# Performance work log

Hardware: AMD Instinct MI355X
Metric: run time of the kernel (lower is better)

The kernel has to match this reference:

```python
import jax, jax.numpy as jnp
import numpy as np

WS = 16          # window_size
SHIFT = 8        # shift_size
HEADS = 6
DIM = 180
CONV_SCALE = 0.01
EPS = 1e-5       # LayerNorm eps (torch default)


def _ln(x, g, b):
    mu = jnp.mean(x, -1, keepdims=True)
    var = jnp.mean((x - mu) ** 2, -1, keepdims=True)
    return (x - mu) / jnp.sqrt(var + EPS) * g + b


def _window_partition(x, ws):
    b, h, w, c = x.shape
    x = x.reshape(b, h // ws, ws, w // ws, ws, c)
    return x.transpose(0, 1, 3, 2, 4, 5).reshape(-1, ws, ws, c)


def _window_reverse(win, ws, h, w):
    b = win.shape[0] // ((h // ws) * (w // ws))
    x = win.reshape(b, h // ws, w // ws, ws, ws, -1)
    return x.transpose(0, 1, 3, 2, 4, 5).reshape(b, h, w, -1)


def _conv2d(x, w, b, pad):
    y = jax.lax.conv_general_dilated(x, w, (1, 1), ((pad, pad), (pad, pad)),
                                     dimension_numbers=('NCHW', 'OIHW', 'NCHW'))
    return y + b[None, :, None, None]


def setup_inputs() -> dict:
    key = jax.random.key(0)
    ks = jax.random.split(key, 12)
    b, h, w = 1, 256, 256
    c = DIM
    hid = int(c * 4.0)
    cr = c // 3     # compress_ratio=3
    sq = c // 30    # squeeze_factor=30
    x = jax.random.normal(ks[0], (b, h * w, c), jnp.float32)

    # relative position index (standard Swin recipe)
    coords = np.stack(np.meshgrid(np.arange(WS), np.arange(WS), indexing='ij')).reshape(2, -1)
    rel = (coords[:, :, None] - coords[:, None, :]).transpose(1, 2, 0)
    rel[:, :, 0] += WS - 1
    rel[:, :, 1] += WS - 1
    rel[:, :, 0] *= 2 * WS - 1
    rpi_sa = jnp.asarray(rel.sum(-1), jnp.int32)  # [ws*ws, ws*ws]

    # shifted-window attention mask
    img = np.zeros((h, w))
    cnt = 0
    for hs in (slice(0, -WS), slice(-WS, -SHIFT), slice(-SHIFT, None)):
        for wsl in (slice(0, -WS), slice(-WS, -SHIFT), slice(-SHIFT, None)):
            img[hs, wsl] = cnt
            cnt += 1
    mw = img.reshape(h // WS, WS, w // WS, WS).transpose(0, 2, 1, 3).reshape(-1, WS * WS)
    am = mw[:, None, :] - mw[:, :, None]
    attn_mask = jnp.asarray(np.where(am != 0, -100.0, 0.0), jnp.float32)  # [nW, n, n]

    def p(k, shape, std=0.02):
        return jax.random.normal(k, shape, jnp.float32) * std

    return dict(
        x=x, h=h, w=w, rpi_sa=rpi_sa, attn_mask=attn_mask,
        norm1_g=jnp.ones((c,), jnp.float32), norm1_b=jnp.zeros((c,), jnp.float32),
        qkv_w=p(ks[1], (c, 3 * c)), qkv_b=jnp.zeros((3 * c,), jnp.float32),
        rpb_table=p(ks[2], ((2 * WS - 1) * (2 * WS - 1), HEADS)),
        proj_w=p(ks[3], (c, c)), proj_b=jnp.zeros((c,), jnp.float32),
        conv1_w=p(ks[4], (cr, c, 3, 3)), conv1_b=jnp.zeros((cr,), jnp.float32),
        conv2_w=p(ks[5], (c, cr, 3, 3)), conv2_b=jnp.zeros((c,), jnp.float32),
        ca1_w=p(ks[6], (sq, c, 1, 1)), ca1_b=jnp.zeros((sq,), jnp.float32),
        ca2_w=p(ks[7], (c, sq, 1, 1)), ca2_b=jnp.zeros((c,), jnp.float32),
        norm2_g=jnp.ones((c,), jnp.float32), norm2_b=jnp.zeros((c,), jnp.float32),
        fc1_w=p(ks[8], (c, hid)), fc1_b=jnp.zeros((hid,), jnp.float32),
        fc2_w=p(ks[9], (hid, c)), fc2_b=jnp.zeros((c,), jnp.float32),
    )


def reference(x, h, w, rpi_sa, attn_mask,
              norm1_g, norm1_b, qkv_w, qkv_b, rpb_table, proj_w, proj_b,
              conv1_w, conv1_b, conv2_w, conv2_b, ca1_w, ca1_b, ca2_w, ca2_b,
              norm2_g, norm2_b, fc1_w, fc1_b, fc2_w, fc2_b):
    b, _, c = x.shape
    shortcut = x
    xn = _ln(x, norm1_g, norm1_b).reshape(b, h, w, c)

    # CAB conv branch (NCHW)
    xi = xn.transpose(0, 3, 1, 2)
    y = _conv2d(xi, conv1_w, conv1_b, 1)
    y = jax.nn.gelu(y, approximate=False)
    y = _conv2d(y, conv2_w, conv2_b, 1)
    ca = jnp.mean(y, axis=(2, 3), keepdims=True)          # AdaptiveAvgPool2d(1)
    ca = jax.nn.relu(_conv2d(ca, ca1_w, ca1_b, 0))
    ca = jax.nn.sigmoid(_conv2d(ca, ca2_w, ca2_b, 0))
    conv_x = (y * ca).transpose(0, 2, 3, 1).reshape(b, h * w, c)

    # shifted window attention
    sx = jnp.roll(xn, (-SHIFT, -SHIFT), (1, 2))
    xw = _window_partition(sx, WS).reshape(-1, WS * WS, c)  # [B_, n, c]
    B_, n, _ = xw.shape
    hd = c // HEADS
    qkv = (xw @ qkv_w + qkv_b).reshape(B_, n, 3, HEADS, hd).transpose(2, 0, 3, 1, 4)
    q, k, v = qkv[0] * hd ** (-0.5), qkv[1], qkv[2]
    attn = jnp.einsum('bhqd,bhkd->bhqk', q, k)
    rpb = rpb_table[rpi_sa.reshape(-1)].reshape(n, n, HEADS).transpose(2, 0, 1)
    attn = attn + rpb[None]
    nw = attn_mask.shape[0]
    attn = attn.reshape(B_ // nw, nw, HEADS, n, n) + attn_mask[None, :, None]
    attn = jax.nn.softmax(attn.reshape(B_, HEADS, n, n), -1)
    out = jnp.einsum('bhqk,bhkd->bhqd', attn, v).transpose(0, 2, 1, 3).reshape(B_, n, c)
    out = out @ proj_w + proj_b
    sx = _window_reverse(out.reshape(-1, WS, WS, c), WS, h, w)
    attn_x = jnp.roll(sx, (SHIFT, SHIFT), (1, 2)).reshape(b, h * w, c)

    x = shortcut + attn_x + conv_x * CONV_SCALE
    xm = _ln(x, norm2_g, norm2_b)
    m = jax.nn.gelu(xm @ fc1_w + fc1_b, approximate=False)
    x = x + (m @ fc2_w + fc2_b)
    return x
```

## Files before the change

### kernel.cpp

```cpp
#include <hip/hip_runtime.h>
#include <hip/hip_bf16.h>
#include <math.h>

#define NTOK 65536
#define C 180
#define KP1 192
#define RCHUNK 32768
#define LOG2E 1.4426950408889634f

typedef __attribute__((ext_vector_type(8))) __bf16 bf16x8;
typedef __attribute__((ext_vector_type(4))) float floatx4;

__device__ __forceinline__ float gelu_f(float v) {
    return 0.5f * v * (1.f + erff(v * 0.7071067811865475f));
}
__device__ __forceinline__ float bflo(unsigned int u) { return __uint_as_float(u << 16); }
__device__ __forceinline__ float bfhi(unsigned int u) { return __uint_as_float(u & 0xffff0000u); }

__device__ __forceinline__ void async_copy16(const unsigned short* g, unsigned short* l) {
    __builtin_amdgcn_global_load_lds(
        (const __attribute__((address_space(1))) unsigned int*)g,
        (__attribute__((address_space(3))) unsigned int*)l, 16, 0, 0);
}

__device__ __forceinline__ int win2pix(int wrow) {
    int wi = wrow >> 8, ni = wrow & 255;
    int r2 = ((wi >> 4) << 4) | (ni >> 4);
    int c2 = ((wi & 15) << 4) | (ni & 15);
    int r = (r2 + 8) & 255, c = (c2 + 8) & 255;
    return (r << 8) | c;
}

__global__ __launch_bounds__(256) void ln_k(const float* __restrict__ x,
                                            const float* __restrict__ g,
                                            const float* __restrict__ b,
                                            __hip_bfloat16* __restrict__ y) {
    const int wav = threadIdx.x >> 6;
    const int lane = threadIdx.x & 63;
    const int row = blockIdx.x * 4 + wav;
    const float* xr = x + (size_t)row * C;
    float v0 = xr[lane];
    float v1 = xr[lane + 64];
    float v2 = (lane < C - 128) ? xr[lane + 128] : 0.f;
    float sum = v0 + v1 + v2;
    float sq = v0 * v0 + v1 * v1 + v2 * v2;
#pragma unroll
    for (int off = 32; off >= 1; off >>= 1) {
        sum += __shfl_xor(sum, off, 64);
        sq += __shfl_xor(sq, off, 64);
    }
    const float mu = sum * (1.f / C);
    const float var = sq * (1.f / C) - mu * mu;
    const float rstd = rsqrtf(var + 1e-5f);
    __hip_bfloat16* yr = y + (size_t)row * KP1;
#pragma unroll
    for (int e = 0; e < 3; ++e) {
        int col = lane + 64 * e;
        float val = 0.f;
        if (col < C) {
            float vv = (e == 0) ? v0 : (e == 1 ? v1 : v2);
            val = (vv - mu) * rstd * g[col] + b[col];
        }
        yr[col] = __float2bfloat16(val);
    }
}

__device__ __forceinline__ void wconv_item(const float* __restrict__ w,
                                           __hip_bfloat16* __restrict__ wb,
                                           int O, int I, int OCP, int KP, int idx) {
    int tap = idx / (OCP * KP);
    int rem = idx - tap * (OCP * KP);
    int oc = rem / KP, ch = rem - oc * KP;
    float v = (oc < O && ch < I) ? w[((size_t)(oc * I + ch)) * 9 + tap] : 0.f;
    wb[idx] = __float2bfloat16(v);
}
__device__ __forceinline__ void wprep_item(const float* __restrict__ w,
                                           __hip_bfloat16* __restrict__ bt,
                                           int K, int N, int KPd, int idx) {
    int n = idx / KPd, k = idx - n * KPd;
    float v = (n < N && k < K) ? w[(size_t)k * N + n] : 0.f;
    bt[idx] = __float2bfloat16(v);
}
__global__ void prep_all_k(const int* __restrict__ rpi, const float* __restrict__ table,
                           const float* __restrict__ mask,
                           __hip_bfloat16* __restrict__ rpbM,
                           const float* __restrict__ c1w, __hip_bfloat16* __restrict__ wb1,
                           const float* __restrict__ c2w, __hip_bfloat16* __restrict__ wb2,
                           const float* __restrict__ qkvw, __hip_bfloat16* __restrict__ qkvbt,
                           const float* __restrict__ projw, __hip_bfloat16* __restrict__ projbt,
                           const float* __restrict__ f1w, __hip_bfloat16* __restrict__ f1bt,
                           const float* __restrict__ f2w, __hip_bfloat16* __restrict__ f2bt) {
    int idx = blockIdx.x * 256 + threadIdx.x;
    if (idx < 65536) {
        int t = rpi[idx];
        float m1 = mask[(size_t)15 * 65536 + idx];
        float m2 = mask[(size_t)240 * 65536 + idx];
        float m3 = mask[(size_t)255 * 65536 + idx];
#pragma unroll
        for (int h = 0; h < 6; ++h) {
            float base = table[t * 6 + h];
            rpbM[((size_t)(0 * 6 + h)) * 65536 + idx] = __float2bfloat16(base * LOG2E);
            rpbM[((size_t)(1 * 6 + h)) * 65536 + idx] = __float2bfloat16((base + m1) * LOG2E);
            rpbM[((size_t)(2 * 6 + h)) * 65536 + idx] = __float2bfloat16((base + m2) * LOG2E);
            rpbM[((size_t)(3 * 6 + h)) * 65536 + idx] = __float2bfloat16((base + m3) * LOG2E);
        }
        return;
    }
    idx -= 65536;
    if (idx < 110592) { wconv_item(c1w, wb1, 60, 180, 64, 192, idx); return; }
    idx -= 110592;
    if (idx < 110592) { wconv_item(c2w, wb2, 180, 60, 192, 64, idx); return; }
    idx -= 110592;
    if (idx < 122880) { wprep_item(qkvw, qkvbt, 180, 540, 192, idx); return; }
    idx -= 122880;
    if (idx < 36864) { wprep_item(projw, projbt, 180, 180, 192, idx); return; }
    idx -= 36864;
    if (idx < 147456) { wprep_item(f1w, f1bt, 180, 720, 192, idx); return; }
    idx -= 147456;
    if (idx < 147456) { wprep_item(f2w, f2bt, 720, 180, 768, idx); return; }
}

template <int TH, int CINP, int COUT, int OSTR, int ACT, int OUTBF>
__global__ __launch_bounds__(256) void mconv_k(const __hip_bfloat16* __restrict__ in, int istr,
                                               const __hip_bfloat16* __restrict__ wb,
                                               const float* __restrict__ bias,
                                               void* __restrict__ outp) {
    constexpr int MI = TH / 4;
    __shared__ __hip_bfloat16 sP[(TH + 2) * 18 * 40];
    __shared__ __hip_bfloat16 sW[9 * 64 * 40];
    const int tid = threadIdx.x;
    const int tr0 = (blockIdx.x >> 4) * TH, tc0 = (blockIdx.x & 15) * 16;
    const int ocbase = blockIdx.y * 64;
    const int w = tid >> 6, lane = tid & 63, fr = lane & 15, q = lane >> 4;
    constexpr int OCP = ((COUT + 63) / 64) * 64;
    floatx4 acc[MI][4] = {};
    for (int c0 = 0; c0 < CINP; c0 += 32) {
        for (int l = tid; l < (TH + 2) * 18 * 4; l += 256) {
            int pos = l >> 2, part = l & 3;
            int pr = pos / 18, pc = pos - pr * 18;
            int gr = tr0 + pr - 1, gc = tc0 + pc - 1;
            float4 v = make_float4(0.f, 0.f, 0.f, 0.f);
            if (gr >= 0 && gr < 256 && gc >= 0 && gc < 256)
                v = *(const float4*)(in + (size_t)(gr * 256 + gc) * istr + c0 + part * 8);
            *(float4*)(sP + pos * 40 + part * 8) = v;
        }
        for (int l = tid; l < 9 * 64 * 4; l += 256) {
            int part = l & 3, oc = (l >> 2) & 63, tap = l >> 8;
            *(float4*)(sW + tap * 2560 + oc * 40 + part * 8) =
                *(const float4*)(wb + (size_t)(tap * OCP + ocbase + oc) * CINP + c0 + part * 8);
        }
        __syncthreads();
#pragma unroll
        for (int tap = 0; tap < 9; ++tap) {
            const int dy = tap / 3, dx = tap - 3 * (tap / 3);
            bf16x8 af[MI], bw[4];
#pragma unroll
            for (int mi = 0; mi < MI; ++mi) {
                int pr = MI * w + mi + dy, pc = fr + dx;
                af[mi] = *(const bf16x8*)(sP + (pr * 18 + pc) * 40 + q * 8);
            }
#pragma unroll
            for (int nj = 0; nj < 4; ++nj)
                bw[nj] = *(const bf16x8*)(sW + tap * 2560 + (nj * 16 + fr) * 40 + q * 8);
#pragma unroll
            for (int mi = 0; mi < MI; ++mi)
#pragma unroll
                for (int nj = 0; nj < 4; ++nj)
                    acc[mi][nj] =
                        __builtin_amdgcn_mfma_f32_16x16x32_bf16(af[mi], bw[nj], acc[mi][nj], 0, 0, 0);
        }
        __syncthreads();
    }
#pragma unroll
    for (int mi = 0; mi < MI; ++mi) {
#pragma unroll
        for (int r = 0; r < 4; ++r) {
            const int irow = tr0 + MI * w + mi;
            const int icol = tc0 + q * 4 + r;
            const size_t obase = (size_t)(irow * 256 + icol) * OSTR + ocbase;
#pragma unroll
            for (int nj = 0; nj < 4; ++nj) {
                int oc = ocbase + nj * 16 + fr;
                float bv = (oc < COUT) ? bias[oc] : 0.f;
                float v = acc[mi][nj][r] + bv;
                if (ACT) v = gelu_f(v);
                if (OUTBF) {
                    ((__hip_bfloat16*)outp)[obase + nj * 16 + fr] = __float2bfloat16(v);
                } else {
                    if (oc < COUT) ((float*)outp)[obase + nj * 16 + fr] = v;
                }
            }
        }
    }
}

__global__ __launch_bounds__(192) void chansum_k(const float* __restrict__ y2,
                                                 float* __restrict__ partials) {
    const int tid = threadIdx.x;
    if (tid >= C) return;
    const size_t base = (size_t)blockIdx.x * 256 * C;
    float s = 0.f;
    for (int p = 0; p < 256; ++p) s += y2[base + (size_t)p * C + tid];
    partials[blockIdx.x * C + tid] = s;
}

__global__ __launch_bounds__(256) void ca_k(const float* __restrict__ partials,
                                            const float* __restrict__ w1, const float* __restrict__ b1,
                                            const float* __restrict__ w2, const float* __restrict__ b2,
                                            float* __restrict__ scale) {
    __shared__ float mean[C];
    __shared__ float s1[6];
    const int tid = threadIdx.x;
    if (tid < C) {
        float s = 0.f;
        for (int b_ = 0; b_ < 256; ++b_) s += partials[b_ * C + tid];
        mean[tid] = s * (1.f / 65536.f);
    }
    __syncthreads();
    if (tid < 6) {
        float s = b1[tid];
        for (int ch = 0; ch < C; ++ch) s += mean[ch] * w1[tid * C + ch];
        s1[tid] = fmaxf(s, 0.f);
    }
    __syncthreads();
    if (tid < C) {
        float s = b2[tid];
#pragma unroll
        for (int j = 0; j < 6; ++j) s += s1[j] * w2[tid * 6 + j];
        scale[tid] = 1.f / (1.f + __expf(-s));
    }
}

template <int MODE, int BN>
__global__ __launch_bounds__(256) void mgemm_k(const unsigned short* __restrict__ A,
                                               const unsigned short* __restrict__ BT,
                                               const float* __restrict__ bias,
                                               const float* __restrict__ xres,
                                               const float* __restrict__ scale,
                                               void* __restrict__ Cout,
                                               int KPd, int N, int cstride, int rowoff) {
    __shared__ unsigned short As[128 * 32];
    __shared__ unsigned short Bs[BN * 32];
    constexpr int NJ = BN / 32;
    const int tid = threadIdx.x;
    const int m0 = blockIdx.x * 128, n0 = blockIdx.y * BN;
    const int wave = tid >> 6, lane = tid & 63;
    const int wm = (wave & 1) * 64, wn = (wave >> 1) * (BN / 2);
    const int fr = lane & 15, q = lane >> 4;
    const int subrow = lane >> 2;
    const int chunk = (lane & 3) ^ (subrow & 3);

    const int rl0 = wave * 16 + subrow;
    const int rl1 = (wave + 4) * 16 + subrow;
    size_t abase0, abase1;
    if (MODE == 3) {
        abase0 = (size_t)win2pix(rowoff + m0 + rl0) * KPd + chunk * 8;
        abase1 = (size_t)win2pix(rowoff + m0 + rl1) * KPd + chunk * 8;
    } else if (MODE == 5) {
        abase0 = (size_t)(m0 + rl0) * 32 + chunk * 8;
        abase1 = (size_t)(m0 + rl1) * 32 + chunk * 8;
    } else {
        abase0 = (size_t)(m0 + rl0) * KPd + chunk * 8;
        abase1 = (size_t)(m0 + rl1) * KPd + chunk * 8;
    }
    const size_t bbase0 = (size_t)(n0 + rl0) * KPd + chunk * 8;
    const size_t bbase1 = (size_t)(n0 + rl1) * KPd + chunk * 8;

    floatx4 acc[4][NJ] = {};
    for (int k0 = 0; k0 < KPd; k0 += 32) {
        if (MODE == 5) {
            const size_t kofs = (size_t)(k0 >> 5) * cstride * 32;
            async_copy16(A + kofs + abase0, As + wave * 512);
            async_copy16(A + kofs + abase1, As + (wave + 4) * 512);
        } else {
            async_copy16(A + abase0 + k0, As + wave * 512);
            async_copy16(A + abase1 + k0, As + (wave + 4) * 512);
        }
        async_copy16(BT + bbase0 + k0, Bs + wave * 512);
        if (BN == 128) async_copy16(BT + bbase1 + k0, Bs + (wave + 4) * 512);
        __syncthreads();
        bf16x8 af[4], fB[NJ];
        const int sw = (q ^ (fr & 3)) << 4;
#pragma unroll
        for (int i = 0; i < 4; ++i)
            af[i] = *(const bf16x8*)((const char*)As + (wm + i * 16 + fr) * 64 + sw);
#pragma unroll
        for (int j = 0; j < NJ; ++j)
            fB[j] = *(const bf16x8*)((const char*)Bs + (wn + j * 16 + fr) * 64 + sw);
#pragma unroll
        for (int i = 0; i < 4; ++i)
#pragma unroll
            for (int j = 0; j < NJ; ++j)
                acc[i][j] = __builtin_amdgcn_mfma_f32_16x16x32_bf16(af[i], fB[j], acc[i][j], 0, 0, 0);
        __syncthreads();
    }
#pragma unroll
    for (int i = 0; i < 4; ++i) {
#pragma unroll
        for (int r = 0; r < 4; ++r) {
            const int grow = m0 + wm + i * 16 + q * 4 + r;
            int pix = 0;
            if (MODE == 5) pix = win2pix(rowoff + grow);
#pragma unroll
            for (int j = 0; j < NJ; ++j) {
                const int col = n0 + wn + j * 16 + fr;
                float v = acc[i][j][r];
                if (MODE == 1 || MODE == 3) {
                    if (col < cstride) {
                        float vv = 0.f;
                        if (col < N) {
                            vv = v + bias[col];
                            if (MODE == 1) vv = gelu_f(vv);
                        }
                        ((__hip_bfloat16*)Cout)[(size_t)grow * cstride + col] = __float2bfloat16(vv);
                    }
                } else if (MODE == 2) {
                    if (col < N) {
                        float* o = (float*)Cout;
                        size_t ix = (size_t)grow * 180 + col;
                        o[ix] = v + bias[col] + xres[ix];
                    }
                } else if (MODE == 5) {
                    if (col < N) {
                        float* o = (float*)Cout;
                        size_t ix = (size_t)pix * 180 + col;
                        o[ix] = xres[ix] + v + bias[col] + o[ix] * scale[col] * 0.01f;
                    }
                }
            }
        }
    }
}

__global__ __launch_bounds__(256, 4) void attn12_k(const __hip_bfloat16* __restrict__ qkv,
                                                   const __hip_bfloat16* __restrict__ rpbM,
                                                   __hip_bfloat16* __restrict__ attn_out,
                                                   int wbase, int rows) {
    const int wl = blockIdx.x, h = blockIdx.y;
    const int wig = wbase + wl;
    const int typ = (((wig >> 4) == 15) ? 2 : 0) + (((wig & 15) == 15) ? 1 : 0);
    const int tid = threadIdx.x;
    const int w = tid >> 6, lane = tid & 63;
    const int fr = lane & 15, q = lane >> 4;
    __shared__ __hip_bfloat16 kk[256 * 32];
    __shared__ __hip_bfloat16 vT[32 * 256];

    union UB2 { unsigned int u; __hip_bfloat162 h2; };
    union U8 { unsigned int u[4]; bf16x8 v; };

    const int rowbase = wl * 256 + w * 64;
    bf16x8 qf[4];
#pragma unroll
    for (int qi = 0; qi < 4; ++qi) {
        const unsigned int* p32 =
            (const unsigned int*)(qkv + (size_t)(rowbase + qi * 16 + fr) * 576 + h * 30);
        U8 t;
#pragma unroll
        for (int jj = 0; jj < 4; ++jj) t.u[jj] = p32[q * 4 + jj];
        qf[qi] = t.v;
    }

    const __hip_bfloat16* rpbh = rpbM + ((size_t)(typ * 6 + h)) * 65536;
    uint2 rb[4][4];
#pragma unroll
    for (int qi = 0; qi < 4; ++qi) {
        const size_t qoff = ((size_t)(w * 64 + qi * 16 + fr)) * 256 + q * 4;
#pragma unroll
        for (int ki = 0; ki < 4; ++ki)
            rb[qi][ki] = *(const uint2*)(rpbh + qoff + ki * 16);
    }

    for (int l = tid; l < 256 * 15; l += 256) {
        int key = l / 15, dw_ = l - key * 15;
        const unsigned int* ks =
            (const unsigned int*)(qkv + (size_t)(wl * 256 + key) * 576 + 180 + h * 30);
        unsigned int kv = ks[dw_];
        *(unsigned int*)((char*)kk + key * 64 + (((dw_ >> 2) ^ (key & 3)) << 4) + ((dw_ & 3) << 2)) = kv;
        UB2 vv; vv.u = ks[90 + dw_];
        const int d0 = 2 * dw_, d1 = d0 + 1;
        *(__hip_bfloat16*)((char*)vT + d0 * 512 + (((key >> 3) ^ d0) << 4) + ((key & 7) << 1)) = vv.h2.x;
        *(__hip_bfloat16*)((char*)vT + d1 * 512 + (((key >> 3) ^ d1) << 4) + ((key & 7) << 1)) = vv.h2.y;
    }
    *(unsigned int*)((char*)kk + tid * 64 + ((3 ^ (tid & 3)) << 4) + 12) = 0u;
    for (int l = tid; l < 2 * 256; l += 256) {
        int d = 30 + (l >> 8), key = l & 255;
        *(__hip_bfloat16*)((char*)vT + d * 512 + (((key >> 3) ^ d) << 4) + ((key & 7) << 1)) =
            __float2bfloat16(0.f);
    }
    __syncthreads();

    const float SC2 = 0.26339891239045137f;
    float lsum[4] = {};
    floatx4 o_[4][2] = {};
    const int srcA = fr + ((q & 1) << 5);
    const int srcB = srcA + 16;

#pragma unroll
    for (int nc = 0; nc < 4; ++nc) {
        if (nc > 0) {
#pragma unroll
            for (int qi = 0; qi < 4; ++qi) {
                const size_t qoff = ((size_t)(w * 64 + qi * 16 + fr)) * 256 + nc * 64 + q * 4;
#pragma unroll
                for (int ki = 0; ki < 4; ++ki)
                    rb[qi][ki] = *(const uint2*)(rpbh + qoff + ki * 16);
            }
        }
        bf16x8 kf[4];
#pragma unroll
        for (int ki = 0; ki < 4; ++ki) {
            const int key = nc * 64 + ki * 16 + fr;
            kf[ki] = *(const bf16x8*)((const char*)kk + key * 64 + ((q ^ (fr & 3)) << 4));
        }
        unsigned int dw[4][4][2];
#pragma unroll
        for (int qi = 0; qi < 4; ++qi) {
            floatx4 s_[4] = {};
#pragma unroll
            for (int ki = 0; ki < 4; ++ki)
                s_[ki] = __builtin_amdgcn_mfma_f32_16x16x32_bf16(kf[ki], qf[qi], s_[ki], 0, 0, 0);
#pragma unroll
            for (int ki = 0; ki < 4; ++ki) {
                uint2 rbv = rb[qi][ki];
                float b0 = bflo(rbv.x), b1 = bfhi(rbv.x), b2 = bflo(rbv.y), b3 = bfhi(rbv.y);
                float p0 = exp2f(fmaf(s_[ki][0], SC2, b0));
                float p1 = exp2f(fmaf(s_[ki][1], SC2, b1));
                float p2 = exp2f(fmaf(s_[ki][2], SC2, b2));
                float p3 = exp2f(fmaf(s_[ki][3], SC2, b3));
                lsum[qi] += (p0 + p1) + (p2 + p3);
                __hip_bfloat162 lo = {__float2bfloat16(p0), __float2bfloat16(p1)};
                __hip_bfloat162 hi = {__float2bfloat16(p2), __float2bfloat16(p3)};
                UB2 ul, uh; ul.h2 = lo; uh.h2 = hi;
                dw[ki][qi][0] = ul.u;
                dw[ki][qi][1] = uh.u;
            }
        }
#pragma unroll
        for (int kc = 0; kc < 2; ++kc) {
            bf16x8 pa[4];
#pragma unroll
            for (int mi = 0; mi < 4; ++mi) {
                unsigned g0 = __shfl((int)dw[2 * kc][mi][0], srcA, 64);
                unsigned g1 = __shfl((int)dw[2 * kc][mi][1], srcA, 64);
                unsigned g2 = __shfl((int)dw[2 * kc][mi][0], srcB, 64);
                unsigned g3 = __shfl((int)dw[2 * kc][mi][1], srcB, 64);
                unsigned h0 = __shfl((int)dw[2 * kc + 1][mi][0], srcA, 64);
                unsigned h1 = __shfl((int)dw[2 * kc + 1][mi][1], srcA, 64);
                unsigned h2 = __shfl((int)dw[2 * kc + 1][mi][0], srcB, 64);
                unsigned h3 = __shfl((int)dw[2 * kc + 1][mi][1], srcB, 64);
                U8 t;
                const bool lo = (q < 2);
                t.u[0] = lo ? g0 : h0;
                t.u[1] = lo ? g1 : h1;
                t.u[2] = lo ? g2 : h2;
                t.u[3] = lo ? g3 : h3;
                pa[mi] = t.v;
            }
            bf16x8 vb[2];
#pragma unroll
            for (int dj = 0; dj < 2; ++dj) {
                const int d = dj * 16 + fr;
                vb[dj] = *(const bf16x8*)((const char*)vT + d * 512 +
                                          (((nc * 8 + kc * 4 + q) ^ d) << 4));
            }
#pragma unroll
            for (int mi = 0; mi < 4; ++mi)
#pragma unroll
                for (int dj = 0; dj < 2; ++dj)
                    o_[mi][dj] =
                        __builtin_amdgcn_mfma_f32_16x16x32_bf16(pa[mi], vb[dj], o_[mi][dj], 0, 0, 0);
        }
    }
#pragma unroll
    for (int qi = 0; qi < 4; ++qi) {
        lsum[qi] += __shfl_xor(lsum[qi], 16, 64);
        lsum[qi] += __shfl_xor(lsum[qi], 32, 64);
    }
    __hip_bfloat16* plane = attn_out + (size_t)h * rows * 32;
#pragma unroll
    for (int mi = 0; mi < 4; ++mi) {
#pragma unroll
        for (int r = 0; r < 4; ++r) {
            float tot = __shfl(lsum[mi], q * 4 + r, 64);
            float inv = 1.f / tot;
            const int row_local = rowbase + mi * 16 + q * 4 + r;
            __hip_bfloat16* orow = plane + (size_t)row_local * 32;
#pragma unroll
            for (int dj = 0; dj < 2; ++dj) {
                int d = dj * 16 + fr;
                float val = (d < 30) ? o_[mi][dj][r] * inv : 0.f;
                orow[d] = __float2bfloat16(val);
            }
        }
    }
}

extern "C" void kernel_launch(void* const* d_in, const int* in_sizes, int n_in, void* d_out,
                              int out_size, void* d_ws, size_t ws_size, hipStream_t stream) {
    (void)in_sizes; (void)n_in; (void)out_size;
    const float* x = (const float*)d_in[0];
    const int* rpi = (const int*)d_in[3];
    const float* mask = (const float*)d_in[4];
    const float* n1g = (const float*)d_in[5];
    const float* n1b = (const float*)d_in[6];
    const float* qkvw = (const float*)d_in[7];
    const float* qkvb = (const float*)d_in[8];
    const float* rpbt = (const float*)d_in[9];
    const float* projw = (const float*)d_in[10];
    const float* projb = (const float*)d_in[11];
    const float* c1w = (const float*)d_in[12];
    const float* c1b = (const float*)d_in[13];
    const float* c2w = (const float*)d_in[14];
    const float* c2b = (const float*)d_in[15];
    const float* ca1w = (const float*)d_in[16];
    const float* ca1b = (const float*)d_in[17];
    const float* ca2w = (const float*)d_in[18];
    const float* ca2b = (const float*)d_in[19];
    const float* n2g = (const float*)d_in[20];
    const float* n2b = (const float*)d_in[21];
    const float* f1w = (const float*)d_in[22];
    const float* f1b = (const float*)d_in[23];
    const float* f2w = (const float*)d_in[24];
    const float* f2b = (const float*)d_in[25];

    float* ws = (float*)d_ws;
    float* out = (float*)d_out;

    const int merged = (ws_size >= 130511616ull) ? 1 : 0;
    const int RATT = merged ? 65536 : 32768;
    const int nck = merged ? 1 : 2;
    const size_t bufCf = merged ? 25165824u : 12582912u;
    const size_t attnCoff = merged ? 18874368u : 9437184u;

    float* xn_f     = ws;
    float* bufC     = xn_f + 6291456;
    float* partials = bufC + bufCf;
    float* scalep   = partials + 46080;
    float* rpbM_f   = scalep + 192;
    float* wb1_f    = rpbM_f + 786432;
    float* wb2_f    = wb1_f + 55296;
    float* qkvbt_f  = wb2_f + 55296;
    float* projbt_f = qkvbt_f + 61440;
    float* f1bt_f   = projbt_f + 18432;
    float* f2bt_f   = f1bt_f + 73728;

    __hip_bfloat16* xn    = (__hip_bfloat16*)xn_f;
    __hip_bfloat16* y1b   = (__hip_bfloat16*)bufC;
    __hip_bfloat16* qkvC  = (__hip_bfloat16*)bufC;
    __hip_bfloat16* attnC = (__hip_bfloat16*)(bufC + attnCoff);
    __hip_bfloat16* h1    = (__hip_bfloat16*)bufC;
    __hip_bfloat16* rpbM   = (__hip_bfloat16*)rpbM_f;
    __hip_bfloat16* wb1    = (__hip_bfloat16*)wb1_f;
    __hip_bfloat16* wb2    = (__hip_bfloat16*)wb2_f;
    __hip_bfloat16* qkvbt  = (__hip_bfloat16*)qkvbt_f;
    __hip_bfloat16* projbt = (__hip_bfloat16*)projbt_f;
    __hip_bfloat16* f1bt   = (__hip_bfloat16*)f1bt_f;
    __hip_bfloat16* f2bt   = (__hip_bfloat16*)f2bt_f;

    prep_all_k<<<(741376 + 255) / 256, 256, 0, stream>>>(rpi, rpbt, mask, rpbM, c1w, wb1, c2w, wb2,
                                                         qkvw, qkvbt, projw, projbt,
                                                         f1w, f1bt, f2w, f2bt);

    ln_k<<<NTOK / 4, 256, 0, stream>>>(x, n1g, n1b, xn);

    mconv_k<8, 192, 60, 64, 1, 1><<<dim3(512, 1), 256, 0, stream>>>(xn, 192, wb1, c1b, y1b);
    mconv_k<16, 64, 180, 180, 0, 0><<<dim3(256, 3), 256, 0, stream>>>(y1b, 64, wb2, c2b, out);
    chansum_k<<<256, 192, 0, stream>>>(out, partials);
    ca_k<<<1, 256, 0, stream>>>(partials, ca1w, ca1b, ca2w, ca2b, scalep);

    for (int ck = 0; ck < nck; ++ck) {
        const int rowoff = ck * RATT;
        mgemm_k<3, 128><<<dim3(RATT / 128, 5), 256, 0, stream>>>(
            (const unsigned short*)xn, (const unsigned short*)qkvbt, qkvb, nullptr, nullptr,
            qkvC, 192, 540, 576, rowoff);
        attn12_k<<<dim3(RATT / 256, 6), 256, 0, stream>>>(qkvC, rpbM, attnC, rowoff / 256, RATT);
        mgemm_k<5, 64><<<dim3(RATT / 128, 3), 256, 0, stream>>>(
            (const unsigned short*)attnC, (const unsigned short*)projbt, projb, x, scalep,
            out, 192, 180, RATT, rowoff);
    }

    ln_k<<<NTOK / 4, 256, 0, stream>>>(out, n2g, n2b, xn);

    const int nmlp = merged ? 1 : 2;
    const int RM = merged ? NTOK : RCHUNK;
    for (int ck = 0; ck < nmlp; ++ck) {
        const int rowoff = ck * RM;
        mgemm_k<1, 128><<<dim3(RM / 128, 6), 256, 0, stream>>>(
            (const unsigned short*)(xn + (size_t)rowoff * KP1), (const unsigned short*)f1bt,
            f1b, nullptr, nullptr, h1, 192, 720, 768, 0);
        mgemm_k<2, 64><<<dim3(RM / 128, 3), 256, 0, stream>>>(
            (const unsigned short*)h1, (const unsigned short*)f2bt, f2b,
            out + (size_t)rowoff * 180, nullptr, out + (size_t)rowoff * 180, 768, 180, 180, 0);
    }
}
```

Baseline: 686.9 us.

## Fuse MLP fc1+GELU+fc2 into one kernel keeping hidden tile in LDS

Replaces the two MLP GEMM launches (fc1 with GELU writing a 65536x768 bf16 hidden buffer, then fc2 with residual) with a single fused kernel. Each 128-row block loads its normalized input tile into LDS, computes 128-column hidden chunks with GELU into an LDS buffer, and accumulates fc2 directly, so the hidden activation never touches global memory. In exchange, the grid shrinks to 512 blocks with large LDS use (about 80KB) and heavy register use for two accumulator sets. Weight fragments are read straight from global memory with no LDS staging, which may stall the MFMA pipeline.

```diff
diff --git a/kernel.cpp b/kernel.cpp
--- a/kernel.cpp
+++ b/kernel.cpp
@@ -5,7 +5,6 @@
 #define NTOK 65536
 #define C 180
 #define KP1 192
-#define RCHUNK 32768
 #define LOG2E 1.4426950408889634f
 
 typedef __attribute__((ext_vector_type(8))) __bf16 bf16x8;
@@ -305,20 +304,11 @@
             for (int j = 0; j < NJ; ++j) {
                 const int col = n0 + wn + j * 16 + fr;
                 float v = acc[i][j][r];
-                if (MODE == 1 || MODE == 3) {
+                if (MODE == 3) {
                     if (col < cstride) {
                         float vv = 0.f;
-                        if (col < N) {
-                            vv = v + bias[col];
-                            if (MODE == 1) vv = gelu_f(vv);
-                        }
+                        if (col < N) vv = v + bias[col];
                         ((__hip_bfloat16*)Cout)[(size_t)grow * cstride + col] = __float2bfloat16(vv);
-                    }
-                } else if (MODE == 2) {
-                    if (col < N) {
-                        float* o = (float*)Cout;
-                        size_t ix = (size_t)grow * 180 + col;
-                        o[ix] = v + bias[col] + xres[ix];
                     }
                 } else if (MODE == 5) {
                     if (col < N) {
@@ -326,6 +316,111 @@
                         size_t ix = (size_t)pix * 180 + col;
                         o[ix] = xres[ix] + v + bias[col] + o[ix] * scale[col] * 0.01f;
                     }
+                }
+            }
+        }
+    }
+}
+
+__global__ __launch_bounds__(256, 2) void mlp_k(const unsigned short* __restrict__ A,
+                                                const unsigned short* __restrict__ B1,
+                                                const float* __restrict__ b1,
+                                                const unsigned short* __restrict__ B2,
+                                                const float* __restrict__ b2,
+                                                float* __restrict__ out) {
+    __shared__ unsigned short xs[128 * 192];
+    __shared__ unsigned short hbuf[128 * 128];
+    const int tid = threadIdx.x;
+    const int m0 = blockIdx.x * 128;
+    const int wave = tid >> 6, lane = tid & 63;
+    const int fr = lane & 15, q = lane >> 4;
+    const int wm = (wave & 1) * 64;
+    const int wn1 = (wave >> 1) * 64;
+    const int wn2 = (wave >> 1) * 96;
+
+    for (int t = 0; t < 12; ++t) {
+        const int seg = wave * 12 + t;
+        const int ci = seg * 64 + lane;
+        const int row = ci / 24, c = ci - row * 24;
+        async_copy16(A + (size_t)(m0 + row) * 192 + ((c ^ (row & 3)) << 3), xs + seg * 512);
+    }
+    __syncthreads();
+
+    floatx4 acc2[4][6] = {};
+    for (int ch = 0; ch < 6; ++ch) {
+        const int c0 = ch * 128;
+        floatx4 acc1[4][4] = {};
+#pragma unroll
+        for (int kk = 0; kk < 6; ++kk) {
+            bf16x8 af[4], fb[4];
+#pragma unroll
+            for (int i = 0; i < 4; ++i) {
+                const int row = wm + i * 16 + fr;
+                const int c = (kk * 4 + q) ^ (row & 3);
+                af[i] = *(const bf16x8*)((const char*)xs + row * 384 + (c << 4));
+            }
+#pragma unroll
+            for (int j = 0; j < 4; ++j) {
+                const int nh = c0 + wn1 + j * 16 + fr;
+                fb[j] = *(const bf16x8*)(B1 + (size_t)nh * 192 + kk * 32 + q * 8);
+            }
+#pragma unroll
+            for (int i = 0; i < 4; ++i)
+#pragma unroll
+                for (int j = 0; j < 4; ++j)
+                    acc1[i][j] =
+                        __builtin_amdgcn_mfma_f32_16x16x32_bf16(af[i], fb[j], acc1[i][j], 0, 0, 0);
+        }
+#pragma unroll
+        for (int i = 0; i < 4; ++i)
+#pragma unroll
+            for (int j = 0; j < 4; ++j)
+#pragma unroll
+                for (int r = 0; r < 4; ++r) {
+                    const int row = wm + i * 16 + q * 4 + r;
+                    const int col = wn1 + j * 16 + fr;
+                    const int hcol = c0 + col;
+                    float v = acc1[i][j][r] + ((hcol < 720) ? b1[hcol] : 0.f);
+                    v = gelu_f(v);
+                    *(__hip_bfloat16*)((char*)hbuf + row * 256 +
+                                       (((col >> 3) ^ (row & 3)) << 4) + ((col & 7) << 1)) =
+                        __float2bfloat16(v);
+                }
+        __syncthreads();
+#pragma unroll
+        for (int kk = 0; kk < 4; ++kk) {
+            bf16x8 af[4], fb[6];
+#pragma unroll
+            for (int i = 0; i < 4; ++i) {
+                const int row = wm + i * 16 + fr;
+                const int c = (kk * 4 + q) ^ (row & 3);
+                af[i] = *(const bf16x8*)((const char*)hbuf + row * 256 + (c << 4));
+            }
+#pragma unroll
+            for (int j = 0; j < 6; ++j) {
+                const int n = wn2 + j * 16 + fr;
+                fb[j] = *(const bf16x8*)(B2 + (size_t)n * 768 + c0 + kk * 32 + q * 8);
+            }
+#pragma unroll
+            for (int i = 0; i < 4; ++i)
+#pragma unroll
+                for (int j = 0; j < 6; ++j)
+                    acc2[i][j] =
+                        __builtin_amdgcn_mfma_f32_16x16x32_bf16(af[i], fb[j], acc2[i][j], 0, 0, 0);
+        }
+        __syncthreads();
+    }
+#pragma unroll
+    for (int i = 0; i < 4; ++i) {
+#pragma unroll
+        for (int r = 0; r < 4; ++r) {
+            const int grow = m0 + wm + i * 16 + q * 4 + r;
+#pragma unroll
+            for (int j = 0; j < 6; ++j) {
+                const int col = wn2 + j * 16 + fr;
+                if (col < 180) {
+                    size_t ix = (size_t)grow * 180 + col;
+                    out[ix] = acc2[i][j][r] + b2[col] + out[ix];
                 }
             }
         }
@@ -548,7 +643,6 @@
     __hip_bfloat16* y1b   = (__hip_bfloat16*)bufC;
     __hip_bfloat16* qkvC  = (__hip_bfloat16*)bufC;
     __hip_bfloat16* attnC = (__hip_bfloat16*)(bufC + attnCoff);
-    __hip_bfloat16* h1    = (__hip_bfloat16*)bufC;
     __hip_bfloat16* rpbM   = (__hip_bfloat16*)rpbM_f;
     __hip_bfloat16* wb1    = (__hip_bfloat16*)wb1_f;
     __hip_bfloat16* wb2    = (__hip_bfloat16*)wb2_f;
@@ -581,15 +675,6 @@
 
     ln_k<<<NTOK / 4, 256, 0, stream>>>(out, n2g, n2b, xn);
 
-    const int nmlp = merged ? 1 : 2;
-    const int RM = merged ? NTOK : RCHUNK;
-    for (int ck = 0; ck < nmlp; ++ck) {
-        const int rowoff = ck * RM;
-        mgemm_k<1, 128><<<dim3(RM / 128, 6), 256, 0, stream>>>(
-            (const unsigned short*)(xn + (size_t)rowoff * KP1), (const unsigned short*)f1bt,
-            f1b, nullptr, nullptr, h1, 192, 720, 768, 0);
-        mgemm_k<2, 64><<<dim3(RM / 128, 3), 256, 0, stream>>>(
-            (const unsigned short*)h1, (const unsigned short*)f2bt, f2b,
-            out + (size_t)rowoff * 180, nullptr, out + (size_t)rowoff * 180, 768, 180, 180, 0);
-    }
-}
+    mlp_k<<<512, 256, 0, stream>>>((const unsigned short*)xn, (const unsigned short*)f1bt, f1b,
+                                   (const unsigned short*)f2bt, f2b, out);
+}
```

Result: slower. 755.5 us (+10.0%).
